# Kernel tuning notes

Hardware: AMD Instinct MI355X
Metric: run time of the kernel (lower is better)

## Reference

```python
import jax, jax.numpy as jnp
import numpy as np

B, C, H, W = 4, 128, 64, 64
EPS = 1e-5


def _mvn(x):
    # per-sample, per-channel mean/std over spatial dims; torch .var() is unbiased (ddof=1)
    m = x.mean(axis=(2, 3), keepdims=True)
    v = x.var(axis=(2, 3), keepdims=True, ddof=1) + EPS
    return (x - m) / jnp.sqrt(v)


def _conv1x1(x, w, b=None):
    # w: [O, C] (squeezed 1x1 kernel)
    y = jnp.einsum('bchw,oc->bohw', x, w)
    if b is not None:
        y = y + b[None, :, None, None]
    return y


def setup_inputs() -> dict:
    key = jax.random.key(0)
    ks = jax.random.split(key, 10)
    s = 1.0 / np.sqrt(C)
    d = {
        'content': jax.random.normal(ks[0], (B, C, H, W), jnp.float32),
        'guidance': jax.random.normal(ks[1], (B, C, H, W), jnp.float32),
        'g1_w': jax.random.normal(ks[2], (C, C), jnp.float32) * s,
        'g1_b': jnp.zeros((C,), jnp.float32),
        'f_w': jax.random.normal(ks[3], (C, C), jnp.float32) * s,
        'f_b': jnp.zeros((C,), jnp.float32),
        'h_w': jax.random.normal(ks[4], (C, C), jnp.float32) * s,
        'h_b': jnp.zeros((C,), jnp.float32),
        # gamma/beta are overwritten in __init__ to shape (1, C, 1, 1) filled with 1e-4
        'gamma_w': jnp.full((C,), 1e-4, jnp.float32),
        'beta_w': jnp.full((C,), 1e-4, jnp.float32),
        'out_w': jax.random.normal(ks[5], (C, C), jnp.float32) * s,
        'out_b': jnp.zeros((C,), jnp.float32),
    }
    return d


def reference(content, guidance, g1_w, g1_b, f_w, f_b, h_w, h_b, gamma_w, beta_w, out_w, out_b):
    b, c, h, w = guidance.shape
    hw = h * w
    G1 = _conv1x1(_mvn(content), g1_w, g1_b)          # [b,c,h,w]
    Fm = _conv1x1(_mvn(guidance), f_w, f_b)           # [b,c,h,w]
    Hm = _conv1x1(guidance, h_w, h_b)                 # [b,c,h,w]

    Ff = Fm.reshape(b, c, hw).transpose(0, 2, 1)      # [b,hw,c]
    G1f = G1.reshape(b, c, hw)                        # [b,c,hw]
    Atten = jax.nn.softmax(jnp.einsum('bnc,bcm->bnm', Ff, G1f), axis=-1)  # [b,hw,hw]

    Hf = Hm.reshape(b, c, hw)                         # [b,c,hw]
    # torch.bmm(H, Atten^T): sum over Atten row index m
    G2 = jax.nn.softmax(jnp.einsum('bcm,bnm->bcn', Hf, Atten), axis=-1)   # [b,c,hw]

    G1r = G1f.reshape(b, c, h, w)
    G2r = G2.reshape(b, c, h, w)
    # gamma/beta convs have weight [1,C,1,1] -> single-output-channel channel sum
    gamma = jnp.einsum('bchw,c->bhw', G2r, gamma_w)[:, None]  # [b,1,h,w]
    beta = jnp.einsum('bchw,c->bhw', G2r, beta_w)[:, None]    # [b,1,h,w]

    Out = jnp.matmul(G1r, gamma) + beta               # [h,w]@[h,w] needs h==w
    return _conv1x1(Out, out_w, out_b)
```

## Files before the change

kernel.cpp:

```cpp
#include <hip/hip_runtime.h>
#include <stdint.h>
#include <stddef.h>

#define BB 4
#define CC 128
#define HWN 4096
#define LOG2E 1.4426950408889634f

typedef __bf16 bf16x2 __attribute__((ext_vector_type(2)));
typedef __bf16 bf16x8 __attribute__((ext_vector_type(8)));
typedef float f32x16 __attribute__((ext_vector_type(16)));

__device__ __forceinline__ void g2l16(void* lds_ptr, const void* gptr) {
  __builtin_amdgcn_global_load_lds(
      (const __attribute__((address_space(1))) uint32_t*)gptr,
      (__attribute__((address_space(3))) uint32_t*)lds_ptr,
      16, 0, 0);
}

__device__ __forceinline__ int p16(int x) {
  return ((x & 4) << 1) | ((x & 8) >> 1) | (x & 3);
}

__global__ __launch_bounds__(128) void w2prep_kernel(
    const float* __restrict__ outw, const float* __restrict__ g1w,
    const float* __restrict__ g1b, float* __restrict__ W2, float* __restrict__ b2) {
  int o = blockIdx.x;
  int c = threadIdx.x;
  float acc = 0.f;
#pragma unroll 8
  for (int k = 0; k < CC; ++k)
    acc = fmaf(outw[o * CC + k], g1w[k * CC + c], acc);
  W2[o * CC + c] = acc;
  if (c == 0) {
    float s = 0.f;
#pragma unroll 8
    for (int k = 0; k < CC; ++k) s = fmaf(outw[o * CC + k], g1b[k], s);
    b2[o] = s;
  }
}

__global__ __launch_bounds__(256) void moments_kernel(
    const float* __restrict__ content, const float* __restrict__ guidance,
    float2* __restrict__ mom) {
  int row = blockIdx.x;
  const float* x = (blockIdx.y ? guidance : content) + (size_t)row * HWN;
  int tid = threadIdx.x;
  float s1 = 0.f, s2 = 0.f;
#pragma unroll
  for (int i = 0; i < 16; ++i) {
    float v = x[tid + i * 256];
    s1 += v; s2 += v * v;
  }
#pragma unroll
  for (int off = 32; off > 0; off >>= 1) {
    s1 += __shfl_down(s1, off);
    s2 += __shfl_down(s2, off);
  }
  __shared__ float r1[4], r2[4];
  int wid = tid >> 6;
  if ((tid & 63) == 0) { r1[wid] = s1; r2[wid] = s2; }
  __syncthreads();
  if (tid == 0) {
    float t1 = r1[0] + r1[1] + r1[2] + r1[3];
    float t2 = r2[0] + r2[1] + r2[2] + r2[3];
    float mean = t1 * (1.f / HWN);
    float var = (t2 - (float)HWN * mean * mean) * (1.f / (HWN - 1));
    mom[blockIdx.y * (BB * CC) + row] = make_float2(mean, rsqrtf(var + 1e-5f));
  }
}

__global__ __launch_bounds__(128) void wcast_kernel(
    const float* __restrict__ g1w, const float* __restrict__ fw,
    const float* __restrict__ fb, const float* __restrict__ hwt,
    const float* __restrict__ hb, const float* __restrict__ W2f,
    const float2* __restrict__ mom,
    __bf16* __restrict__ WK, __bf16* __restrict__ WQ, __bf16* __restrict__ WT,
    __bf16* __restrict__ WV, float* __restrict__ BqL, float* __restrict__ hb_b) {
  int row = blockIdx.x;
  int y = blockIdx.y;
  int c = threadIdx.x;
  int cp = (c & ~15) | p16(c & 15);
  if (y == 0) {
    WK[row * CC + cp] = (__bf16)g1w[row * CC + c];
  } else if (y == 1) {
    WQ[row * CC + cp] = (__bf16)(fw[row * CC + c] * LOG2E);
    if (c == 0) BqL[row] = fb[row] * LOG2E;
  } else if (y == 2) {
    WT[row * CC + cp] = (__bf16)W2f[row * CC + c];
  } else {
    int b = y - 3;
    float2 ms = mom[BB * CC + b * CC + c];
    WV[((size_t)b * CC + row) * CC + cp] = (__bf16)(hwt[row * CC + c] / ms.y);
    __shared__ float red[128];
    red[c] = hwt[row * CC + c] * ms.x;
    __syncthreads();
#pragma unroll
    for (int off = 64; off > 0; off >>= 1) {
      if (c < off) red[c] += red[c + off];
      __syncthreads();
    }
    if (c == 0) hb_b[b * CC + row] = hb[row] + red[0];
  }
}

__global__ __launch_bounds__(256) void convm_kernel(
    const float* __restrict__ content, const float* __restrict__ guidance,
    const float2* __restrict__ mom,
    const __bf16* __restrict__ WK, const __bf16* __restrict__ WQ,
    const __bf16* __restrict__ WT, const __bf16* __restrict__ WV,
    const float* __restrict__ g1b, const float* __restrict__ b2,
    const float* __restrict__ BqL, const float* __restrict__ hb_b,
    float* __restrict__ Tf, __bf16* __restrict__ QTb, __bf16* __restrict__ KTb,
    __bf16* __restrict__ Vb) {
  __shared__ __align__(16) char lds[65536];
  int z = blockIdx.z;
  int b = blockIdx.y;
  int p0 = blockIdx.x * 128;
  int tid = threadIdx.x;
  int lane = tid & 63, wid = tid >> 6;
  int l31 = lane & 31, h = lane >> 5;
  const float* x = (z < 2 ? content : guidance) + (size_t)b * CC * HWN;
  const float2* mb = mom + (z < 2 ? 0 : BB * CC) + b * CC;
  const __bf16* wsel = (z == 0) ? WK : (z == 1) ? WT : (z == 2) ? WQ
                       : WV + (size_t)b * CC * CC;
  const float* bias = (z == 0) ? g1b : (z == 1) ? b2 : (z == 2) ? BqL
                      : hb_b + b * CC;

  {
    const char* wG = (const char*)wsel;
    char* wl = lds + 32768;
#pragma unroll
    for (int op = 0; op < 8; ++op) {
      int ck = op * 4 + wid;
      int row = ck * 4 + (lane >> 4);
      int u = lane & 15;
      g2l16(wl + (size_t)ck * 1024,
            wG + (size_t)row * 256 + ((u ^ (row & 15)) << 4));
    }
  }
  {
    char* xl = lds;
    int pl = (tid & 63) * 2;
    int c0 = (tid >> 6) * 32;
#pragma unroll 8
    for (int k = 0; k < 32; ++k) {
      int c = c0 + k;
      float2 ms = mb[c];
      float2 v = *(const float2*)(x + (size_t)c * HWN + p0 + pl);
      __bf16 e0 = (__bf16)((v.x - ms.x) * ms.y);
      __bf16 e1 = (__bf16)((v.y - ms.x) * ms.y);
      int cp = (c & ~15) | p16(c & 15);
      int cb = (cp * 2) & 15;
      *(__bf16*)(xl + pl * 256 + ((((cp >> 3) ^ (pl & 15)) << 4) | cb)) = e0;
      *(__bf16*)(xl + (pl + 1) * 256 + ((((cp >> 3) ^ ((pl + 1) & 15)) << 4) | cb)) = e1;
    }
  }
  __syncthreads();

  f32x16 Of[4];
#pragma unroll
  for (int q = 0; q < 4; ++q)
#pragma unroll
    for (int r = 0; r < 16; ++r) Of[q][r] = 0.f;
  const char* xl = lds;
  const char* wl = lds + 32768;
  int xrow = wid * 32 + l31;
#pragma unroll
  for (int j = 0; j < 8; ++j) {
    bf16x8 xf = *(const bf16x8*)(xl + xrow * 256 + (((2 * j + h) ^ (xrow & 15)) << 4));
#pragma unroll
    for (int q = 0; q < 4; ++q) {
      int wrow = q * 32 + l31;
      bf16x8 wf = *(const bf16x8*)(wl + wrow * 256 + (((2 * j + h) ^ (wrow & 15)) << 4));
      Of[q] = __builtin_amdgcn_mfma_f32_32x32x16_bf16(wf, xf, Of[q], 0, 0, 0);
    }
  }

  int p = p0 + wid * 32 + l31;
  if (z == 0 || z == 2) {
    __bf16* T = (z == 0) ? KTb : QTb;
    char* rowp = (char*)(T + ((size_t)b * HWN + p) * CC);
#pragma unroll
    for (int q = 0; q < 4; ++q)
#pragma unroll
      for (int r = 0; r < 16; r += 2) {
        int o = q * 32 + (r & 3) + 8 * (r >> 2) + 4 * h;
        bf16x2 pr = {(__bf16)(Of[q][r] + bias[o]), (__bf16)(Of[q][r + 1] + bias[o + 1])};
        int pp = (o & ~15) | p16(o & 15);
        *(bf16x2*)(rowp + pp * 2) = pr;
      }
  } else if (z == 1) {
#pragma unroll
    for (int q = 0; q < 4; ++q)
#pragma unroll
      for (int r = 0; r < 16; ++r) {
        int o = q * 32 + (r & 3) + 8 * (r >> 2) + 4 * h;
        Tf[((size_t)b * CC + o) * HWN + p] = Of[q][r] + bias[o];
      }
  } else {
    int ws_ = (l31 & 16) | p16(l31 & 15);
    __bf16* tbase = Vb + ((size_t)(b * (HWN / 32) + (p >> 5)) * CC) * 32 + ws_;
#pragma unroll
    for (int q = 0; q < 4; ++q)
#pragma unroll
      for (int r = 0; r < 16; ++r) {
        int o = q * 32 + (r & 3) + 8 * (r >> 2) + 4 * h;
        tbase[(size_t)o * 32] = (__bf16)(Of[q][r] + bias[o]);
      }
  }
}

__global__ __launch_bounds__(512, 2) void attn_kernel(
    const __bf16* __restrict__ QTb, const __bf16* __restrict__ KTb,
    const __bf16* __restrict__ Vb, float* __restrict__ G2p) {
  __shared__ __align__(16) char lds[131072];
  int fid = blockIdx.x;
  int swz = (fid & 7) * 32 + (fid >> 3);
  int b = swz >> 6;
  int ntile = swz & 63;
  int tid = threadIdx.x;
  int lane = tid & 63;
  int wid = tid >> 6;
  int grp = wid >> 1;
  int w2 = wid & 1;
  int l31 = lane & 31;
  int h = lane >> 5;
  int nb = ntile * 64 + w2 * 32;
  char* kslot0 = lds + (size_t)wid * 16384;

  bf16x8 qf[8];
  {
    const char* qrow = (const char*)(QTb + ((size_t)b * HWN + nb + l31) * CC);
#pragma unroll
    for (int i = 0; i < 8; ++i)
      qf[i] = *(const bf16x8*)(qrow + i * 32 + h * 16);
  }

  f32x16 Of[4];
#pragma unroll
  for (int q = 0; q < 4; ++q)
#pragma unroll
    for (int r = 0; r < 16; ++r) Of[q][r] = 0.f;
  float mrun = -1e30f, lrun = 0.f;

  const char* ktB = (const char*)(KTb + (size_t)b * HWN * CC);
  const char* vtB = (const char*)Vb + ((size_t)(b * (HWN / 32) + grp * 32)) * 8192;
  int vlane = l31 * 64 + h * 16;

  auto stage = [&](int i) {
    int m0 = grp * 1024 + i * 32;
    char* buf = kslot0 + (size_t)(i & 1) * 8192;
#pragma unroll
    for (int j = 0; j < 8; ++j) {
      int row = j * 4 + (lane >> 4);
      int chk = (lane & 15) ^ (row & 15);
      g2l16(buf + j * 1024, ktB + (size_t)(m0 + row) * 256 + chk * 16);
    }
  };
  auto loadV = [&](int i, bf16x8 (&vf)[8]) {
    const char* vt = vtB + (size_t)i * 8192;
#pragma unroll
    for (int cs = 0; cs < 4; ++cs)
#pragma unroll
      for (int kk = 0; kk < 2; ++kk)
        vf[cs * 2 + kk] = *(const bf16x8*)(vt + cs * 2048 + kk * 32 + vlane);
  };

  bf16x8 vfA[8], vfB[8];

  auto step = [&](bf16x8 (&useV)[8], bf16x8 (&nextV)[8], int i,
                  bool do_stage, bool do_loadv, bool last) {
    if (last) asm volatile("s_waitcnt vmcnt(8)" ::: "memory");
    else      asm volatile("s_waitcnt vmcnt(16)" ::: "memory");
    if (do_loadv) loadV(i + 1, nextV);
    const char* kt = kslot0 + (size_t)(i & 1) * 8192;
    bf16x8 kf[8];
#pragma unroll
    for (int j = 0; j < 8; ++j) {
      int chk = (2 * j + h) ^ (l31 & 15);
      kf[j] = *(const bf16x8*)(kt + l31 * 256 + chk * 16);
    }
    asm volatile("s_waitcnt lgkmcnt(0)" ::: "memory");
    __builtin_amdgcn_sched_barrier(0);
    if (do_stage) stage(i + 2);

    f32x16 s;
#pragma unroll
    for (int r = 0; r < 16; ++r) s[r] = 0.f;
#pragma unroll
    for (int j = 0; j < 8; ++j)
      s = __builtin_amdgcn_mfma_f32_32x32x16_bf16(kf[j], qf[j], s, 0, 0, 0);
    float tm = s[0];
#pragma unroll
    for (int r = 1; r < 16; ++r) tm = fmaxf(tm, s[r]);
    tm = fmaxf(tm, __shfl_xor(tm, 32));
    if (!__all(tm <= mrun + 8.f)) {
      float mnew = fmaxf(mrun, tm);
      float alpha = exp2f(mrun - mnew);
      lrun *= alpha;
#pragma unroll
      for (int q = 0; q < 4; ++q) Of[q] *= alpha;
      mrun = mnew;
    }
    float ps = 0.f;
    bf16x8 pf0, pf1;
#pragma unroll
    for (int r = 0; r < 16; ++r) {
      float e = exp2f(s[r] - mrun);
      ps += e;
      if (r < 8) pf0[r] = (__bf16)e; else pf1[r - 8] = (__bf16)e;
    }
    ps += __shfl_xor(ps, 32);
    lrun += ps;
#pragma unroll
    for (int cs = 0; cs < 4; ++cs) {
      Of[cs] = __builtin_amdgcn_mfma_f32_32x32x16_bf16(useV[cs * 2],     pf0, Of[cs], 0, 0, 0);
      Of[cs] = __builtin_amdgcn_mfma_f32_32x32x16_bf16(useV[cs * 2 + 1], pf1, Of[cs], 0, 0, 0);
    }
  };

  stage(0);
  stage(1);
  loadV(0, vfA);
#pragma unroll 1
  for (int i = 0; i < 30; i += 2) {
    step(vfA, vfB, i,     true, true, false);
    step(vfB, vfA, i + 1, true, true, false);
  }
  step(vfA, vfB, 30, false, true,  false);
  step(vfB, vfA, 31, false, false, true);

  __syncthreads();
  float* xch = (float*)lds;
  if (grp) {
    float* rec = xch + (size_t)((grp - 1) * 128 + w2 * 64 + lane) * 68;
#pragma unroll
    for (int q = 0; q < 4; ++q)
#pragma unroll
      for (int r = 0; r < 16; ++r) rec[q * 16 + r] = Of[q][r];
    rec[64] = mrun;
    rec[65] = lrun;
  }
  __syncthreads();
  if (grp == 0) {
    const float* r1 = xch + (size_t)(0 * 128 + w2 * 64 + lane) * 68;
    const float* r2 = xch + (size_t)(1 * 128 + w2 * 64 + lane) * 68;
    const float* r3 = xch + (size_t)(2 * 128 + w2 * 64 + lane) * 68;
    float m1 = r1[64], m2 = r2[64], m3 = r3[64];
    float mm = fmaxf(fmaxf(mrun, m1), fmaxf(m2, m3));
    float a0 = exp2f(mrun - mm), a1 = exp2f(m1 - mm);
    float a2 = exp2f(m2 - mm), a3 = exp2f(m3 - mm);
    float inv = 1.f / (lrun * a0 + r1[65] * a1 + r2[65] * a2 + r3[65] * a3);
    float* outp = G2p + (size_t)b * CC * HWN + nb + l31;
#pragma unroll
    for (int q = 0; q < 4; ++q)
#pragma unroll
      for (int r = 0; r < 16; ++r) {
        int c = q * 32 + (r & 3) + 8 * (r >> 2) + 4 * h;
        float v = Of[q][r] * a0 + r1[q * 16 + r] * a1 + r2[q * 16 + r] * a2 + r3[q * 16 + r] * a3;
        outp[(size_t)c * HWN] = v * inv;
      }
  }
}

__global__ __launch_bounds__(256) void smstats_kernel(
    const float* __restrict__ G2p, float2* __restrict__ smst) {
  int row = blockIdx.x;
  const float* x = G2p + (size_t)row * HWN;
  int tid = threadIdx.x;
  float v[16];
  float mx = -1e30f;
#pragma unroll
  for (int i = 0; i < 16; ++i) { v[i] = x[tid + i * 256]; mx = fmaxf(mx, v[i]); }
#pragma unroll
  for (int off = 32; off > 0; off >>= 1) mx = fmaxf(mx, __shfl_xor(mx, off));
  __shared__ float rm[4], rs[4];
  int wid = tid >> 6;
  if ((tid & 63) == 0) rm[wid] = mx;
  __syncthreads();
  float bmax = fmaxf(fmaxf(rm[0], rm[1]), fmaxf(rm[2], rm[3]));
  float s = 0.f;
#pragma unroll
  for (int i = 0; i < 16; ++i) s += __expf(v[i] - bmax);
#pragma unroll
  for (int off = 32; off > 0; off >>= 1) s += __shfl_xor(s, off);
  if ((tid & 63) == 0) rs[wid] = s;
  __syncthreads();
  if (tid == 0) {
    float tot = rs[0] + rs[1] + rs[2] + rs[3];
    smst[row] = make_float2(bmax, 1.f / tot);
  }
}

__global__ __launch_bounds__(256) void gammabeta_kernel(
    const float* __restrict__ G2p, const float2* __restrict__ smst,
    const float* __restrict__ gw, const float* __restrict__ bw,
    float* __restrict__ gamma, float* __restrict__ beta) {
  int b = blockIdx.y;
  int lane = threadIdx.x & 63;
  int cg = threadIdx.x >> 6;
  int m = blockIdx.x * 64 + lane;
  const float* base = G2p + (size_t)b * CC * HWN + m;
  float ag = 0.f, ab = 0.f;
#pragma unroll 8
  for (int ci = 0; ci < 32; ++ci) {
    int c = cg * 32 + ci;
    float2 st = smst[b * CC + c];
    float val = __expf(base[(size_t)c * HWN] - st.x) * st.y;
    ag = fmaf(gw[c], val, ag);
    ab = fmaf(bw[c], val, ab);
  }
  __shared__ float sg[4][64], sb[4][64];
  sg[cg][lane] = ag;
  sb[cg][lane] = ab;
  __syncthreads();
  if (threadIdx.x < 64) {
    int t = threadIdx.x;
    gamma[b * HWN + blockIdx.x * 64 + t] = sg[0][t] + sg[1][t] + sg[2][t] + sg[3][t];
    beta[b * HWN + blockIdx.x * 64 + t]  = sb[0][t] + sb[1][t] + sb[2][t] + sb[3][t];
  }
}

__global__ __launch_bounds__(256) void final_kernel(
    const float* __restrict__ Tf, const float* __restrict__ gamma,
    const float* __restrict__ beta, const float* __restrict__ outw,
    const float* __restrict__ outb, float* __restrict__ out) {
  int o = blockIdx.x, b = blockIdx.y;
  int j = threadIdx.x & 63;
  int wid = __builtin_amdgcn_readfirstlane(threadIdx.x >> 6);
  const float* gb_ = gamma + (size_t)b * HWN;
  float gr[64];
#pragma unroll
  for (int k = 0; k < 64; ++k) gr[k] = gb_[k * 64 + j];
  float wb = 0.f;
#pragma unroll 16
  for (int c = 0; c < CC; ++c) wb += outw[o * CC + c];
  float ob = outb[o];
  const float* trow0 = Tf + ((size_t)b * CC + o) * HWN;
  const float* bbase = beta + (size_t)b * HWN;
  float* obase = out + ((size_t)b * CC + o) * HWN;
#pragma unroll 4
  for (int r = 0; r < 16; ++r) {
    int i = r * 4 + wid;
    const float* tr = trow0 + i * 64;
    float a0 = 0.f, a1 = 0.f, a2 = 0.f, a3 = 0.f;
#pragma unroll
    for (int k = 0; k < 64; k += 4) {
      a0 = fmaf(tr[k],     gr[k],     a0);
      a1 = fmaf(tr[k + 1], gr[k + 1], a1);
      a2 = fmaf(tr[k + 2], gr[k + 2], a2);
      a3 = fmaf(tr[k + 3], gr[k + 3], a3);
    }
    obase[i * 64 + j] = (a0 + a1) + (a2 + a3) + wb * bbase[i * 64 + j] + ob;
  }
}

extern "C" void kernel_launch(void* const* d_in, const int* in_sizes, int n_in,
                              void* d_out, int out_size, void* d_ws, size_t ws_size,
                              hipStream_t stream) {
  (void)in_sizes; (void)n_in; (void)out_size; (void)ws_size;
  const float* content  = (const float*)d_in[0];
  const float* guidance = (const float*)d_in[1];
  const float* g1w = (const float*)d_in[2];
  const float* g1b = (const float*)d_in[3];
  const float* fw  = (const float*)d_in[4];
  const float* fb  = (const float*)d_in[5];
  const float* hwt = (const float*)d_in[6];
  const float* hb  = (const float*)d_in[7];
  const float* gw  = (const float*)d_in[8];
  const float* bw  = (const float*)d_in[9];
  const float* outw = (const float*)d_in[10];
  const float* outb = (const float*)d_in[11];

  char* ws = (char*)d_ws;
  const size_t MB_ = 1u << 20;
  float*  Tf  = (float*)(ws + 0);
  float*  G2p = (float*)(ws + 8 * MB_);
  __bf16* QTb = (__bf16*)(ws + 16 * MB_);
  __bf16* KTb = (__bf16*)(ws + 20 * MB_);
  __bf16* Vb  = (__bf16*)(ws + 24 * MB_);
  float2* mom  = (float2*)(ws + 28 * MB_);
  float2* smst = (float2*)(ws + 28 * MB_ + 8192);
  float*  gamma = (float*)(ws + 28 * MB_ + 16384);
  float*  beta  = (float*)(ws + 28 * MB_ + 16384 + 65536);
  float*  W2f = (float*)(ws + 28 * MB_ + 16384 + 2 * 65536);
  float*  b2  = (float*)(ws + 28 * MB_ + 16384 + 3 * 65536);
  char*   wb_ = ws + 28 * MB_ + 16384 + 3 * 65536 + 1024;
  __bf16* WK = (__bf16*)(wb_);
  __bf16* WQ = (__bf16*)(wb_ + 32768);
  __bf16* WT = (__bf16*)(wb_ + 65536);
  __bf16* WV = (__bf16*)(wb_ + 98304);
  float*  BqL  = (float*)(wb_ + 98304 + 131072);
  float*  hb_b = (float*)(wb_ + 98304 + 131072 + 512);

  moments_kernel<<<dim3(BB * CC, 2), 256, 0, stream>>>(content, guidance, mom);
  w2prep_kernel<<<dim3(CC), 128, 0, stream>>>(outw, g1w, g1b, W2f, b2);
  wcast_kernel<<<dim3(CC, 7), 128, 0, stream>>>(
      g1w, fw, fb, hwt, hb, W2f, mom, WK, WQ, WT, WV, BqL, hb_b);
  convm_kernel<<<dim3(HWN / 128, BB, 4), 256, 0, stream>>>(
      content, guidance, mom, WK, WQ, WT, WV, g1b, b2, BqL, hb_b,
      Tf, QTb, KTb, Vb);
  attn_kernel<<<dim3(256), 512, 0, stream>>>(QTb, KTb, Vb, G2p);
  smstats_kernel<<<dim3(BB * CC), 256, 0, stream>>>(G2p, smst);
  gammabeta_kernel<<<dim3(HWN / 64, BB), 256, 0, stream>>>(G2p, smst, gw, bw, gamma, beta);
  final_kernel<<<dim3(CC, BB), 256, 0, stream>>>(Tf, gamma, beta, outw, outb, (float*)d_out);
}
```

Baseline: 118.1 us.

## Software-pipeline PV MFMAs across iterations and split QK accumulation chains

```diff
diff --git a/kernel.cpp b/kernel.cpp
--- a/kernel.cpp
+++ b/kernel.cpp
@@ -243,6 +243,7 @@
 #pragma unroll
     for (int r = 0; r < 16; ++r) Of[q][r] = 0.f;
   float mrun = -1e30f, lrun = 0.f;
+  bf16x8 pfp0, pfp1;
 
   const char* ktB = (const char*)(KTb + (size_t)b * HWN * CC);
   const char* vtB = (const char*)Vb + ((size_t)(b * (HWN / 32) + grp * 32)) * 8192;
@@ -269,11 +270,18 @@
 
   bf16x8 vfA[8], vfB[8];
 
-  auto step = [&](bf16x8 (&useV)[8], bf16x8 (&nextV)[8], int i,
-                  bool do_stage, bool do_loadv, bool last) {
+  auto step = [&](bf16x8 (&prevV)[8], int i,
+                  bool do_stage, bool do_loadv, bool do_pv, bool last) {
     if (last) asm volatile("s_waitcnt vmcnt(8)" ::: "memory");
     else      asm volatile("s_waitcnt vmcnt(16)" ::: "memory");
-    if (do_loadv) loadV(i + 1, nextV);
+    if (do_pv) {
+#pragma unroll
+      for (int cs = 0; cs < 4; ++cs) {
+        Of[cs] = __builtin_amdgcn_mfma_f32_32x32x16_bf16(prevV[cs * 2],     pfp0, Of[cs], 0, 0, 0);
+        Of[cs] = __builtin_amdgcn_mfma_f32_32x32x16_bf16(prevV[cs * 2 + 1], pfp1, Of[cs], 0, 0, 0);
+      }
+    }
+    if (do_loadv) loadV(i + 1, prevV);
     const char* kt = kslot0 + (size_t)(i & 1) * 8192;
     bf16x8 kf[8];
 #pragma unroll
@@ -285,12 +293,15 @@
     __builtin_amdgcn_sched_barrier(0);
     if (do_stage) stage(i + 2);
 
-    f32x16 s;
-#pragma unroll
-    for (int r = 0; r < 16; ++r) s[r] = 0.f;
-#pragma unroll
-    for (int j = 0; j < 8; ++j)
-      s = __builtin_amdgcn_mfma_f32_32x32x16_bf16(kf[j], qf[j], s, 0, 0, 0);
+    f32x16 sa, sb;
+#pragma unroll
+    for (int r = 0; r < 16; ++r) { sa[r] = 0.f; sb[r] = 0.f; }
+#pragma unroll
+    for (int j = 0; j < 8; j += 2) {
+      sa = __builtin_amdgcn_mfma_f32_32x32x16_bf16(kf[j],     qf[j],     sa, 0, 0, 0);
+      sb = __builtin_amdgcn_mfma_f32_32x32x16_bf16(kf[j + 1], qf[j + 1], sb, 0, 0, 0);
+    }
+    f32x16 s = sa + sb;
     float tm = s[0];
 #pragma unroll
     for (int r = 1; r < 16; ++r) tm = fmaxf(tm, s[r]);
@@ -304,32 +315,33 @@
       mrun = mnew;
     }
     float ps = 0.f;
-    bf16x8 pf0, pf1;
 #pragma unroll
     for (int r = 0; r < 16; ++r) {
       float e = exp2f(s[r] - mrun);
       ps += e;
-      if (r < 8) pf0[r] = (__bf16)e; else pf1[r - 8] = (__bf16)e;
+      if (r < 8) pfp0[r] = (__bf16)e; else pfp1[r - 8] = (__bf16)e;
     }
     ps += __shfl_xor(ps, 32);
     lrun += ps;
-#pragma unroll
-    for (int cs = 0; cs < 4; ++cs) {
-      Of[cs] = __builtin_amdgcn_mfma_f32_32x32x16_bf16(useV[cs * 2],     pf0, Of[cs], 0, 0, 0);
-      Of[cs] = __builtin_amdgcn_mfma_f32_32x32x16_bf16(useV[cs * 2 + 1], pf1, Of[cs], 0, 0, 0);
-    }
   };
 
   stage(0);
   stage(1);
   loadV(0, vfA);
+  step(vfB, 0, true, true, false, false);
+  step(vfA, 1, true, true, true,  false);
 #pragma unroll 1
-  for (int i = 0; i < 30; i += 2) {
-    step(vfA, vfB, i,     true, true, false);
-    step(vfB, vfA, i + 1, true, true, false);
-  }
-  step(vfA, vfB, 30, false, true,  false);
-  step(vfB, vfA, 31, false, false, true);
+  for (int i = 2; i < 30; i += 2) {
+    step(vfB, i,     true, true, true, false);
+    step(vfA, i + 1, true, true, true, false);
+  }
+  step(vfB, 30, false, true,  true, false);
+  step(vfA, 31, false, false, true, true);
+#pragma unroll
+  for (int cs = 0; cs < 4; ++cs) {
+    Of[cs] = __builtin_amdgcn_mfma_f32_32x32x16_bf16(vfB[cs * 2],     pfp0, Of[cs], 0, 0, 0);
+    Of[cs] = __builtin_amdgcn_mfma_f32_32x32x16_bf16(vfB[cs * 2 + 1], pfp1, Of[cs], 0, 0, 0);
+  }
 
   __syncthreads();
   float* xch = (float*)lds;
```

Result: slower. 123.6 us (+4.7%).
